# Kernel optimization log

Measured on AMD Instinct MI355X. Metric: run time of the kernel, lower is better.

The kernel has to match this reference:

```python
import jax, jax.numpy as jnp
import numpy as np

B, N, E, D_IN, D_OUT = 8, 8192, 131072, 128, 128
LN_EPS = 1e-5

def setup_inputs() -> dict:
    key = jax.random.key(0)
    k1, k2, k3, k4 = jax.random.split(key, 4)
    node_features = jax.random.normal(k1, (B, N, D_IN), dtype=jnp.float32)
    edge_index = jax.random.randint(k2, (B, 2, E), 0, N, dtype=jnp.int64)
    node_mask = jnp.ones((B, N), dtype=jnp.float32)
    # Linear params (torch Linear: y = x @ W.T + b)
    W = jax.random.normal(k3, (D_OUT, D_IN), dtype=jnp.float32) / np.sqrt(D_IN)
    b = jax.random.normal(k4, (D_OUT,), dtype=jnp.float32) * 0.01
    # LayerNorm params
    gamma = jnp.ones((D_OUT,), dtype=jnp.float32)
    beta = jnp.zeros((D_OUT,), dtype=jnp.float32)
    return {"node_features": node_features, "edge_index": edge_index,
            "node_mask": node_mask, "W": W, "b": b, "gamma": gamma, "beta": beta}

def reference(node_features, edge_index, node_mask, W, b, gamma, beta):
    max_nodes = node_features.shape[1]
    h = jnp.einsum('bni,oi->bno', node_features, W) + b  # [B,N,D_OUT]
    def agg_one(hb, eb):
        # gather source features then scatter-add into targets
        return jax.ops.segment_sum(hb[eb[0]], eb[1], num_segments=max_nodes)
    aggregated = jax.vmap(agg_one)(h, edge_index)  # [B,N,D_OUT]
    h = h + aggregated / jnp.sqrt(jnp.float32(max_nodes))
    # dropout is identity in eval mode
    mu = jnp.mean(h, axis=-1, keepdims=True)
    var = jnp.mean((h - mu) ** 2, axis=-1, keepdims=True)
    h = (h - mu) * jax.lax.rsqrt(var + LN_EPS) * gamma + beta
    h = jax.nn.relu(h)
    return h * node_mask[..., None]
```

## Files before the change

kernel.cpp:

```cpp
#include <hip/hip_runtime.h>

#define B_ 8
#define N_ 8192
#define E_ 131072
#define D_ 128
#define M_ (B_ * N_)
#define SLOTS 64
#define NCH 32
#define CHE (E_ / NCH)
constexpr float INV_SQRT_N = 0.011048543456039806f;
constexpr float LN_EPS_C = 1e-5f;

typedef __attribute__((ext_vector_type(8))) short bf16x8;
typedef __attribute__((ext_vector_type(4))) float f32x4;
typedef __attribute__((ext_vector_type(4))) float f32x4v;
typedef __attribute__((ext_vector_type(4))) unsigned u32x4;

static __device__ __forceinline__ unsigned short f2bf(float f) {
  unsigned u = __float_as_uint(f);
  u += 0x7fffu + ((u >> 16) & 1u);
  return (unsigned short)(u >> 16);
}
static __device__ __forceinline__ float bflo(unsigned u) {
  return __uint_as_float(u << 16);
}
static __device__ __forceinline__ float bfhi(unsigned u) {
  return __uint_as_float(u & 0xffff0000u);
}
static __device__ __forceinline__ bf16x8 cvt8v(const f32x4v a, const f32x4v b) {
  bf16x8 r;
  r[0] = (short)f2bf(a.x); r[1] = (short)f2bf(a.y);
  r[2] = (short)f2bf(a.z); r[3] = (short)f2bf(a.w);
  r[4] = (short)f2bf(b.x); r[5] = (short)f2bf(b.y);
  r[6] = (short)f2bf(b.z); r[7] = (short)f2bf(b.w);
  return r;
}

__global__ __launch_bounds__(256, 2) void gemm_count_kernel(
    const float* __restrict__ X, const float* __restrict__ W,
    const float* __restrict__ bias, const int* __restrict__ eidx,
    unsigned short* __restrict__ histc, unsigned short* __restrict__ rankb,
    unsigned short* __restrict__ hb) {
  __shared__ unsigned hist[N_];
  if (blockIdx.x < 256) {
    const int wave = threadIdx.x >> 6;
    const int lane = threadIdx.x & 63;
    const int m16 = lane & 15;
    const int q = lane >> 4;
    const int hf = wave & 1;
    const int ng = wave >> 1;

    bf16x8 wf[4][4];
#pragma unroll
    for (int kt4 = 0; kt4 < 4; ++kt4) {
#pragma unroll
      for (int tt = 0; tt < 4; ++tt) {
        const float* wr = W + (size_t)(hf * 64 + tt * 16 + m16) * D_ +
                          kt4 * 32 + q * 8;
        wf[kt4][tt] = cvt8v(*(const f32x4v*)wr, *(const f32x4v*)(wr + 4));
      }
    }

    const int bi = blockIdx.x;
    const int nbase0 = (bi & 7) * N_ + (bi >> 3) * 256 + ng * 128;
#pragma unroll 2
    for (int s = 0; s < 8; ++s) {
      const int nbase = nbase0 + s * 16;
      const float* xrow = X + (size_t)(nbase + m16) * D_;

      f32x4 acc[4];
#pragma unroll
      for (int tt = 0; tt < 4; ++tt) acc[tt] = (f32x4){0.f, 0.f, 0.f, 0.f};

#pragma unroll
      for (int kt4 = 0; kt4 < 4; ++kt4) {
        const f32x4v xa = __builtin_nontemporal_load(
            (const f32x4v*)(xrow + kt4 * 32 + q * 8));
        const f32x4v xb = __builtin_nontemporal_load(
            (const f32x4v*)(xrow + kt4 * 32 + q * 8 + 4));
        const bf16x8 xf = cvt8v(xa, xb);
#pragma unroll
        for (int tt = 0; tt < 4; ++tt) {
          acc[tt] = __builtin_amdgcn_mfma_f32_16x16x32_bf16(wf[kt4][tt], xf,
                                                            acc[tt], 0, 0, 0);
        }
      }

      const size_t orow = (size_t)(nbase + m16) * D_;
#pragma unroll
      for (int tt = 0; tt < 4; ++tt) {
        const int f0 = hf * 64 + tt * 16 + q * 4;
        const float4 b4 = *(const float4*)&bias[f0];
        uint2 uu;
        uu.x = (unsigned)f2bf(acc[tt][0] + b4.x) |
               ((unsigned)f2bf(acc[tt][1] + b4.y) << 16);
        uu.y = (unsigned)f2bf(acc[tt][2] + b4.z) |
               ((unsigned)f2bf(acc[tt][3] + b4.w) << 16);
        *(uint2*)(hb + orow + f0) = uu;
      }
    }
  } else {
    const int f = blockIdx.x - 256;
    const int b = f & 7;
    const int c = f >> 3;
    const int t = threadIdx.x;

#pragma unroll
    for (int i = 0; i < N_ / 256; ++i) hist[t + i * 256] = 0u;
    __syncthreads();

    const int* __restrict__ tgtp = eidx + b * 2 * E_ + E_ + c * CHE;
    unsigned short* __restrict__ rnk = rankb + (size_t)b * E_ + c * CHE;
#pragma unroll
    for (int k = 0; k < 4; ++k) {
      const int4 tv = *(const int4*)(tgtp + t * 16 + k * 4);
      const unsigned r0 = atomicAdd(&hist[tv.x], 1u);
      const unsigned r1 = atomicAdd(&hist[tv.y], 1u);
      const unsigned r2 = atomicAdd(&hist[tv.z], 1u);
      const unsigned r3 = atomicAdd(&hist[tv.w], 1u);
      uint2 rr;
      rr.x = (r0 & 0xffffu) | (r1 << 16);
      rr.y = (r2 & 0xffffu) | (r3 << 16);
      *(uint2*)(rnk + t * 16 + k * 4) = rr;
    }
    __syncthreads();

    unsigned* dst = (unsigned*)(histc + ((size_t)b * NCH + c) * N_);
#pragma unroll
    for (int i = 0; i < N_ / 512; ++i) {
      const int j = t + i * 256;
      const unsigned lo = hist[2 * j];
      const unsigned hi = hist[2 * j + 1];
      dst[j] = (lo & 0xffffu) | (hi << 16);
    }
  }
}

__global__ __launch_bounds__(256, 8) void prefix_kernel(
    unsigned short* __restrict__ histc, int* __restrict__ cnt) {
  const int b = blockIdx.x & 7;
  const int nb = blockIdx.x >> 3;
  const int n = nb * 256 + threadIdx.x;
  unsigned short* base = histc + (size_t)b * NCH * N_ + n;
  unsigned short v[NCH];
#pragma unroll
  for (int c = 0; c < NCH; ++c) v[c] = base[(size_t)c * N_];
  unsigned run = 0;
#pragma unroll
  for (int c = 0; c < NCH; ++c) {
    const unsigned x = v[c];
    base[(size_t)c * N_] = (unsigned short)run;
    run += x;
  }
  cnt[b * N_ + n] = (int)run;
}

__global__ __launch_bounds__(256, 8) void place_kernel(
    const int* __restrict__ eidx, const unsigned short* __restrict__ histc,
    const unsigned short* __restrict__ rankb,
    unsigned short* __restrict__ bucket) {
  const int b = blockIdx.x & 7;
  const int pos = blockIdx.x >> 3;
  const int c = pos >> 2;
  const int t = threadIdx.x;
  const int e0 = pos * 1024 + t * 4;

  const int* __restrict__ srcp = eidx + b * 2 * E_;
  const int4 tv = *(const int4*)(srcp + E_ + e0);
  const int4 sv = *(const int4*)(srcp + e0);
  const uint2 rr = *(const uint2*)(rankb + (size_t)b * E_ + e0);
  const unsigned short* __restrict__ basep = histc + ((size_t)b * NCH + c) * N_;
  unsigned short* __restrict__ bkt = bucket + (size_t)b * N_ * SLOTS;

  const unsigned p0 = (unsigned)basep[tv.x] + (rr.x & 0xffffu);
  const unsigned p1 = (unsigned)basep[tv.y] + (rr.x >> 16);
  const unsigned p2 = (unsigned)basep[tv.z] + (rr.y & 0xffffu);
  const unsigned p3 = (unsigned)basep[tv.w] + (rr.y >> 16);
  if (p0 < SLOTS) bkt[(size_t)tv.x * SLOTS + p0] = (unsigned short)sv.x;
  if (p1 < SLOTS) bkt[(size_t)tv.y * SLOTS + p1] = (unsigned short)sv.y;
  if (p2 < SLOTS) bkt[(size_t)tv.z * SLOTS + p2] = (unsigned short)sv.z;
  if (p3 < SLOTS) bkt[(size_t)tv.w * SLOTS + p3] = (unsigned short)sv.w;
}

__global__ __launch_bounds__(256, 8) void gather_finalize_kernel(
    const unsigned short* __restrict__ hb, const unsigned short* __restrict__ bucket,
    const int* __restrict__ cnt, const float* __restrict__ mask,
    const float* __restrict__ gamma, const float* __restrict__ beta,
    float* __restrict__ out) {
  const int bid = blockIdx.x;
  const int batch = bid & 7;
  const int wave = threadIdx.x >> 6;
  const int lane = threadIdx.x & 63;
  const int g = lane >> 4;
  const int c = lane & 15;
  const int r = (bid >> 3) * 16 + wave * 4 + g;
  const int row = batch * N_ + r;

  const u32x4* hub4 = (const u32x4*)hb + (size_t)batch * N_ * 16;

  const int deg = min(cnt[row], SLOTS);
  const uint2 su = *(const uint2*)&bucket[(size_t)row * SLOTS + c * 4];
  const u32x4 ur = hub4[r * 16 + c];
  const float m = mask[row];

  float a[8];
#pragma unroll
  for (int k = 0; k < 8; ++k) a[k] = 0.f;

  for (int jb = 0; jb < deg; jb += 8) {
    const int L = jb >> 2;
    const unsigned w0 = (unsigned)__shfl((int)su.x, L, 16);
    const unsigned w1 = (unsigned)__shfl((int)su.y, L, 16);
    const unsigned w2 = (unsigned)__shfl((int)su.x, L + 1, 16);
    const unsigned w3 = (unsigned)__shfl((int)su.y, L + 1, 16);
    const int idx[8] = {(int)(w0 & 0xffff), (int)(w0 >> 16),
                        (int)(w1 & 0xffff), (int)(w1 >> 16),
                        (int)(w2 & 0xffff), (int)(w2 >> 16),
                        (int)(w3 & 0xffff), (int)(w3 >> 16)};
    u32x4 v[8];
#pragma unroll
    for (int i = 0; i < 8; ++i) {
      const bool val = (jb + i) < deg;
      const int id = val ? idx[i] : 0;
      u32x4 tv = hub4[id * 16 + c];
      if (!val) tv = (u32x4){0u, 0u, 0u, 0u};
      v[i] = tv;
    }
#pragma unroll
    for (int i = 0; i < 8; ++i) {
      a[0] += bflo(v[i].x); a[1] += bfhi(v[i].x);
      a[2] += bflo(v[i].y); a[3] += bfhi(v[i].y);
      a[4] += bflo(v[i].z); a[5] += bfhi(v[i].z);
      a[6] += bflo(v[i].w); a[7] += bfhi(v[i].w);
    }
  }

  float x[8];
  x[0] = bflo(ur.x) + a[0] * INV_SQRT_N;
  x[1] = bfhi(ur.x) + a[1] * INV_SQRT_N;
  x[2] = bflo(ur.y) + a[2] * INV_SQRT_N;
  x[3] = bfhi(ur.y) + a[3] * INV_SQRT_N;
  x[4] = bflo(ur.z) + a[4] * INV_SQRT_N;
  x[5] = bfhi(ur.z) + a[5] * INV_SQRT_N;
  x[6] = bflo(ur.w) + a[6] * INV_SQRT_N;
  x[7] = bfhi(ur.w) + a[7] * INV_SQRT_N;

  float s0 = 0.f, ss = 0.f;
#pragma unroll
  for (int k = 0; k < 8; ++k) {
    s0 += x[k];
    ss += x[k] * x[k];
  }
#pragma unroll
  for (int o = 8; o >= 1; o >>= 1) {
    s0 += __shfl_xor(s0, o, 16);
    ss += __shfl_xor(ss, o, 16);
  }
  const float mu = s0 * (1.f / 128.f);
  float var = ss * (1.f / 128.f) - mu * mu;
  var = var < 0.f ? 0.f : var;
  const float rstd = rsqrtf(var + LN_EPS_C);

  const f32x4v g0 = *((const f32x4v*)gamma + c * 2);
  const f32x4v g1 = *((const f32x4v*)gamma + c * 2 + 1);
  const f32x4v b0 = *((const f32x4v*)beta + c * 2);
  const f32x4v b1 = *((const f32x4v*)beta + c * 2 + 1);

  f32x4v o0, o1;
  o0.x = (x[0] - mu) * rstd * g0.x + b0.x;
  o0.y = (x[1] - mu) * rstd * g0.y + b0.y;
  o0.z = (x[2] - mu) * rstd * g0.z + b0.z;
  o0.w = (x[3] - mu) * rstd * g0.w + b0.w;
  o1.x = (x[4] - mu) * rstd * g1.x + b1.x;
  o1.y = (x[5] - mu) * rstd * g1.y + b1.y;
  o1.z = (x[6] - mu) * rstd * g1.z + b1.z;
  o1.w = (x[7] - mu) * rstd * g1.w + b1.w;
  o0.x = (o0.x > 0.f ? o0.x : 0.f) * m;
  o0.y = (o0.y > 0.f ? o0.y : 0.f) * m;
  o0.z = (o0.z > 0.f ? o0.z : 0.f) * m;
  o0.w = (o0.w > 0.f ? o0.w : 0.f) * m;
  o1.x = (o1.x > 0.f ? o1.x : 0.f) * m;
  o1.y = (o1.y > 0.f ? o1.y : 0.f) * m;
  o1.z = (o1.z > 0.f ? o1.z : 0.f) * m;
  o1.w = (o1.w > 0.f ? o1.w : 0.f) * m;

  f32x4v* op = (f32x4v*)out + (size_t)row * 32 + c * 2;
  __builtin_nontemporal_store(o0, op);
  __builtin_nontemporal_store(o1, op + 1);
}

extern "C" void kernel_launch(void* const* d_in, const int* in_sizes, int n_in,
                              void* d_out, int out_size, void* d_ws,
                              size_t ws_size, hipStream_t stream) {
  const float* X = (const float*)d_in[0];
  const int* eidx = (const int*)d_in[1];
  const float* mask = (const float*)d_in[2];
  const float* W = (const float*)d_in[3];
  const float* bias = (const float*)d_in[4];
  const float* gamma = (const float*)d_in[5];
  const float* beta = (const float*)d_in[6];
  float* out = (float*)d_out;

  unsigned short* hb = (unsigned short*)d_ws;
  unsigned short* bucket = hb + (size_t)M_ * D_;
  int* cnt = (int*)(bucket + (size_t)M_ * SLOTS);
  unsigned short* rankb = (unsigned short*)(cnt + M_);
  unsigned short* histc = (unsigned short*)out;

  gemm_count_kernel<<<512, 256, 0, stream>>>(X, W, bias, eidx, histc, rankb,
                                             hb);
  prefix_kernel<<<256, 256, 0, stream>>>(histc, cnt);
  place_kernel<<<1024, 256, 0, stream>>>(eidx, histc, rankb, bucket);
  gather_finalize_kernel<<<M_ / 16, 256, 0, stream>>>(hb, bucket, cnt, mask,
                                                      gamma, beta, out);
}
```

Measured before the change: 153.6 us.

## Split feature table into column halves and gather each half in separate passes

The GEMM now writes the bf16 hidden features as two column-half planes of 64 features each, and the gather/finalize step becomes two kernels, one per half. The first pass writes partial pre-norm values and LayerNorm sums to workspace, and the second combines them and applies the normalization. The goal is a per-batch gather working set small enough to stay in cache, cutting random-gather traffic to HBM. The cost is an extra launch, reading the bucket indices twice, and a round trip of fp32 intermediates and stats through memory.

```diff
diff --git a/kernel.cpp b/kernel.cpp
--- a/kernel.cpp
+++ b/kernel.cpp
@@ -14,7 +14,6 @@
 typedef __attribute__((ext_vector_type(8))) short bf16x8;
 typedef __attribute__((ext_vector_type(4))) float f32x4;
 typedef __attribute__((ext_vector_type(4))) float f32x4v;
-typedef __attribute__((ext_vector_type(4))) unsigned u32x4;
 
 static __device__ __forceinline__ unsigned short f2bf(float f) {
   unsigned u = __float_as_uint(f);
@@ -63,6 +62,7 @@
 
     const int bi = blockIdx.x;
     const int nbase0 = (bi & 7) * N_ + (bi >> 3) * 256 + ng * 128;
+    unsigned short* __restrict__ hp = hb + (size_t)hf * M_ * 64;
 #pragma unroll 2
     for (int s = 0; s < 8; ++s) {
       const int nbase = nbase0 + s * 16;
@@ -86,7 +86,7 @@
         }
       }
 
-      const size_t orow = (size_t)(nbase + m16) * D_;
+      const size_t prow = (size_t)(nbase + m16) * 64;
 #pragma unroll
       for (int tt = 0; tt < 4; ++tt) {
         const int f0 = hf * 64 + tt * 16 + q * 4;
@@ -96,7 +96,7 @@
                ((unsigned)f2bf(acc[tt][1] + b4.y) << 16);
         uu.y = (unsigned)f2bf(acc[tt][2] + b4.z) |
                ((unsigned)f2bf(acc[tt][3] + b4.w) << 16);
-        *(uint2*)(hb + orow + f0) = uu;
+        *(uint2*)(hp + prow + tt * 16 + q * 4) = uu;
       }
     }
   } else {
@@ -182,11 +182,10 @@
   if (p3 < SLOTS) bkt[(size_t)tv.w * SLOTS + p3] = (unsigned short)sv.w;
 }
 
-__global__ __launch_bounds__(256, 8) void gather_finalize_kernel(
-    const unsigned short* __restrict__ hb, const unsigned short* __restrict__ bucket,
-    const int* __restrict__ cnt, const float* __restrict__ mask,
-    const float* __restrict__ gamma, const float* __restrict__ beta,
-    float* __restrict__ out) {
+__global__ __launch_bounds__(256, 8) void gather_half0_kernel(
+    const unsigned short* __restrict__ hb0,
+    const unsigned short* __restrict__ bucket, const int* __restrict__ cnt,
+    float* __restrict__ xh, float2* __restrict__ stats) {
   const int bid = blockIdx.x;
   const int batch = bid & 7;
   const int wave = threadIdx.x >> 6;
@@ -196,17 +195,13 @@
   const int r = (bid >> 3) * 16 + wave * 4 + g;
   const int row = batch * N_ + r;
 
-  const u32x4* hub4 = (const u32x4*)hb + (size_t)batch * N_ * 16;
+  const uint2* hub2 = (const uint2*)hb0 + (size_t)batch * N_ * 16;
 
   const int deg = min(cnt[row], SLOTS);
   const uint2 su = *(const uint2*)&bucket[(size_t)row * SLOTS + c * 4];
-  const u32x4 ur = hub4[r * 16 + c];
-  const float m = mask[row];
-
-  float a[8];
-#pragma unroll
-  for (int k = 0; k < 8; ++k) a[k] = 0.f;
-
+  const uint2 ur = hub2[r * 16 + c];
+
+  float a[4] = {0.f, 0.f, 0.f, 0.f};
   for (int jb = 0; jb < deg; jb += 8) {
     const int L = jb >> 2;
     const unsigned w0 = (unsigned)__shfl((int)su.x, L, 16);
@@ -217,64 +212,124 @@
                         (int)(w1 & 0xffff), (int)(w1 >> 16),
                         (int)(w2 & 0xffff), (int)(w2 >> 16),
                         (int)(w3 & 0xffff), (int)(w3 >> 16)};
-    u32x4 v[8];
+    uint2 v[8];
 #pragma unroll
     for (int i = 0; i < 8; ++i) {
       const bool val = (jb + i) < deg;
-      const int id = val ? idx[i] : 0;
-      u32x4 tv = hub4[id * 16 + c];
-      if (!val) tv = (u32x4){0u, 0u, 0u, 0u};
+      uint2 tv = hub2[(val ? idx[i] : 0) * 16 + c];
+      if (!val) tv = (uint2){0u, 0u};
       v[i] = tv;
     }
 #pragma unroll
     for (int i = 0; i < 8; ++i) {
       a[0] += bflo(v[i].x); a[1] += bfhi(v[i].x);
       a[2] += bflo(v[i].y); a[3] += bfhi(v[i].y);
-      a[4] += bflo(v[i].z); a[5] += bfhi(v[i].z);
-      a[6] += bflo(v[i].w); a[7] += bfhi(v[i].w);
-    }
-  }
-
-  float x[8];
-  x[0] = bflo(ur.x) + a[0] * INV_SQRT_N;
-  x[1] = bfhi(ur.x) + a[1] * INV_SQRT_N;
-  x[2] = bflo(ur.y) + a[2] * INV_SQRT_N;
-  x[3] = bfhi(ur.y) + a[3] * INV_SQRT_N;
-  x[4] = bflo(ur.z) + a[4] * INV_SQRT_N;
-  x[5] = bfhi(ur.z) + a[5] * INV_SQRT_N;
-  x[6] = bflo(ur.w) + a[6] * INV_SQRT_N;
-  x[7] = bfhi(ur.w) + a[7] * INV_SQRT_N;
-
-  float s0 = 0.f, ss = 0.f;
-#pragma unroll
-  for (int k = 0; k < 8; ++k) {
-    s0 += x[k];
-    ss += x[k] * x[k];
-  }
+    }
+  }
+
+  float4 x;
+  x.x = bflo(ur.x) + a[0] * INV_SQRT_N;
+  x.y = bfhi(ur.x) + a[1] * INV_SQRT_N;
+  x.z = bflo(ur.y) + a[2] * INV_SQRT_N;
+  x.w = bfhi(ur.y) + a[3] * INV_SQRT_N;
+
+  float s0 = x.x + x.y + x.z + x.w;
+  float ss = x.x * x.x + x.y * x.y + x.z * x.z + x.w * x.w;
 #pragma unroll
   for (int o = 8; o >= 1; o >>= 1) {
     s0 += __shfl_xor(s0, o, 16);
     ss += __shfl_xor(ss, o, 16);
   }
+
+  *(float4*)(xh + (size_t)row * 64 + c * 4) = x;
+  if (c == 0) stats[row] = make_float2(s0, ss);
+}
+
+__global__ __launch_bounds__(256, 8) void gather_half1_kernel(
+    const unsigned short* __restrict__ hb1,
+    const unsigned short* __restrict__ bucket, const int* __restrict__ cnt,
+    const float* __restrict__ mask, const float* __restrict__ gamma,
+    const float* __restrict__ beta, const float* __restrict__ xh,
+    const float2* __restrict__ stats, float* __restrict__ out) {
+  const int bid = blockIdx.x;
+  const int batch = bid & 7;
+  const int wave = threadIdx.x >> 6;
+  const int lane = threadIdx.x & 63;
+  const int g = lane >> 4;
+  const int c = lane & 15;
+  const int r = (bid >> 3) * 16 + wave * 4 + g;
+  const int row = batch * N_ + r;
+
+  const uint2* hub2 = (const uint2*)hb1 + (size_t)batch * N_ * 16;
+
+  const int deg = min(cnt[row], SLOTS);
+  const uint2 su = *(const uint2*)&bucket[(size_t)row * SLOTS + c * 4];
+  const uint2 ur = hub2[r * 16 + c];
+  const float m = mask[row];
+
+  float a[4] = {0.f, 0.f, 0.f, 0.f};
+  for (int jb = 0; jb < deg; jb += 8) {
+    const int L = jb >> 2;
+    const unsigned w0 = (unsigned)__shfl((int)su.x, L, 16);
+    const unsigned w1 = (unsigned)__shfl((int)su.y, L, 16);
+    const unsigned w2 = (unsigned)__shfl((int)su.x, L + 1, 16);
+    const unsigned w3 = (unsigned)__shfl((int)su.y, L + 1, 16);
+    const int idx[8] = {(int)(w0 & 0xffff), (int)(w0 >> 16),
+                        (int)(w1 & 0xffff), (int)(w1 >> 16),
+                        (int)(w2 & 0xffff), (int)(w2 >> 16),
+                        (int)(w3 & 0xffff), (int)(w3 >> 16)};
+    uint2 v[8];
+#pragma unroll
+    for (int i = 0; i < 8; ++i) {
+      const bool val = (jb + i) < deg;
+      uint2 tv = hub2[(val ? idx[i] : 0) * 16 + c];
+      if (!val) tv = (uint2){0u, 0u};
+      v[i] = tv;
+    }
+#pragma unroll
+    for (int i = 0; i < 8; ++i) {
+      a[0] += bflo(v[i].x); a[1] += bfhi(v[i].x);
+      a[2] += bflo(v[i].y); a[3] += bfhi(v[i].y);
+    }
+  }
+
+  float4 x1;
+  x1.x = bflo(ur.x) + a[0] * INV_SQRT_N;
+  x1.y = bfhi(ur.x) + a[1] * INV_SQRT_N;
+  x1.z = bflo(ur.y) + a[2] * INV_SQRT_N;
+  x1.w = bfhi(ur.y) + a[3] * INV_SQRT_N;
+
+  float s0 = x1.x + x1.y + x1.z + x1.w;
+  float ss = x1.x * x1.x + x1.y * x1.y + x1.z * x1.z + x1.w * x1.w;
+#pragma unroll
+  for (int o = 8; o >= 1; o >>= 1) {
+    s0 += __shfl_xor(s0, o, 16);
+    ss += __shfl_xor(ss, o, 16);
+  }
+  const float2 st = stats[row];
+  s0 += st.x;
+  ss += st.y;
+
   const float mu = s0 * (1.f / 128.f);
   float var = ss * (1.f / 128.f) - mu * mu;
   var = var < 0.f ? 0.f : var;
   const float rstd = rsqrtf(var + LN_EPS_C);
 
-  const f32x4v g0 = *((const f32x4v*)gamma + c * 2);
-  const f32x4v g1 = *((const f32x4v*)gamma + c * 2 + 1);
-  const f32x4v b0 = *((const f32x4v*)beta + c * 2);
-  const f32x4v b1 = *((const f32x4v*)beta + c * 2 + 1);
+  const float4 x0 = *(const float4*)(xh + (size_t)row * 64 + c * 4);
+  const float4 g0 = ((const float4*)gamma)[c];
+  const float4 g1 = ((const float4*)gamma)[16 + c];
+  const float4 b0 = ((const float4*)beta)[c];
+  const float4 b1 = ((const float4*)beta)[16 + c];
 
   f32x4v o0, o1;
-  o0.x = (x[0] - mu) * rstd * g0.x + b0.x;
-  o0.y = (x[1] - mu) * rstd * g0.y + b0.y;
-  o0.z = (x[2] - mu) * rstd * g0.z + b0.z;
-  o0.w = (x[3] - mu) * rstd * g0.w + b0.w;
-  o1.x = (x[4] - mu) * rstd * g1.x + b1.x;
-  o1.y = (x[5] - mu) * rstd * g1.y + b1.y;
-  o1.z = (x[6] - mu) * rstd * g1.z + b1.z;
-  o1.w = (x[7] - mu) * rstd * g1.w + b1.w;
+  o0.x = (x0.x - mu) * rstd * g0.x + b0.x;
+  o0.y = (x0.y - mu) * rstd * g0.y + b0.y;
+  o0.z = (x0.z - mu) * rstd * g0.z + b0.z;
+  o0.w = (x0.w - mu) * rstd * g0.w + b0.w;
+  o1.x = (x1.x - mu) * rstd * g1.x + b1.x;
+  o1.y = (x1.y - mu) * rstd * g1.y + b1.y;
+  o1.z = (x1.z - mu) * rstd * g1.z + b1.z;
+  o1.w = (x1.w - mu) * rstd * g1.w + b1.w;
   o0.x = (o0.x > 0.f ? o0.x : 0.f) * m;
   o0.y = (o0.y > 0.f ? o0.y : 0.f) * m;
   o0.z = (o0.z > 0.f ? o0.z : 0.f) * m;
@@ -284,9 +339,9 @@
   o1.z = (o1.z > 0.f ? o1.z : 0.f) * m;
   o1.w = (o1.w > 0.f ? o1.w : 0.f) * m;
 
-  f32x4v* op = (f32x4v*)out + (size_t)row * 32 + c * 2;
-  __builtin_nontemporal_store(o0, op);
-  __builtin_nontemporal_store(o1, op + 1);
+  f32x4v* op = (f32x4v*)out + (size_t)row * 32;
+  __builtin_nontemporal_store(o0, op + c);
+  __builtin_nontemporal_store(o1, op + 16 + c);
 }
 
 extern "C" void kernel_launch(void* const* d_in, const int* in_sizes, int n_in,
@@ -302,15 +357,19 @@
   float* out = (float*)d_out;
 
   unsigned short* hb = (unsigned short*)d_ws;
-  unsigned short* bucket = hb + (size_t)M_ * D_;
+  unsigned short* bucket = hb + (size_t)2 * M_ * 64;
   int* cnt = (int*)(bucket + (size_t)M_ * SLOTS);
   unsigned short* rankb = (unsigned short*)(cnt + M_);
+  float* xh = (float*)(rankb + (size_t)B_ * E_);
+  float2* stats = (float2*)(xh + (size_t)M_ * 64);
   unsigned short* histc = (unsigned short*)out;
 
   gemm_count_kernel<<<512, 256, 0, stream>>>(X, W, bias, eidx, histc, rankb,
                                              hb);
   prefix_kernel<<<256, 256, 0, stream>>>(histc, cnt);
   place_kernel<<<1024, 256, 0, stream>>>(eidx, histc, rankb, bucket);
-  gather_finalize_kernel<<<M_ / 16, 256, 0, stream>>>(hb, bucket, cnt, mask,
-                                                      gamma, beta, out);
-}
+  gather_half0_kernel<<<M_ / 16, 256, 0, stream>>>(hb, bucket, cnt, xh, stats);
+  gather_half1_kernel<<<M_ / 16, 256, 0, stream>>>(hb + (size_t)M_ * 64,
+                                                   bucket, cnt, mask, gamma,
+                                                   beta, xh, stats, out);
+}
```

New measurement: 161.9 us. +5.4%, slower.

## Fuse count, prefix and place kernels with grid-wide software barriers

Applied to the files above, without the earlier changes.

Merges the histogram/count, prefix-scan and placement kernels into one launch that also holds the GEMM blocks. The 256 counting blocks synchronise among themselves with atomic-counter spin barriers before the scan and placement phases, and a memset resets the counters beforehand. This removes two kernel launches and the gaps between them. It depends on all 256 counting blocks being co-resident: 512 blocks at 2 per CU with 32KB LDS each could deadlock if residency is insufficient, and the memset adds its own small launch.

```diff
diff --git a/kernel.cpp b/kernel.cpp
--- a/kernel.cpp
+++ b/kernel.cpp
@@ -36,15 +36,34 @@
   return r;
 }
 
-__global__ __launch_bounds__(256, 2) void gemm_count_kernel(
+static __device__ __forceinline__ void sub_barrier(unsigned* bar,
+                                                   unsigned nblk) {
+  __syncthreads();
+  if (threadIdx.x == 0) {
+    __threadfence();
+    atomicAdd(bar, 1u);
+    while (__hip_atomic_load(bar, __ATOMIC_RELAXED,
+                             __HIP_MEMORY_SCOPE_AGENT) < nblk) {
+      __builtin_amdgcn_s_sleep(1);
+    }
+  }
+  __syncthreads();
+  __threadfence();
+}
+
+__global__ __launch_bounds__(256, 2) void fused_front_kernel(
     const float* __restrict__ X, const float* __restrict__ W,
     const float* __restrict__ bias, const int* __restrict__ eidx,
     unsigned short* __restrict__ histc, unsigned short* __restrict__ rankb,
-    unsigned short* __restrict__ hb) {
+    unsigned short* __restrict__ hb, int* __restrict__ cnt,
+    unsigned short* __restrict__ bucket, unsigned* __restrict__ bar) {
   __shared__ unsigned hist[N_];
-  if (blockIdx.x < 256) {
-    const int wave = threadIdx.x >> 6;
-    const int lane = threadIdx.x & 63;
+  const int bid = blockIdx.x;
+  const int t = threadIdx.x;
+
+  if (bid < 256) {
+    const int wave = t >> 6;
+    const int lane = t & 63;
     const int m16 = lane & 15;
     const int q = lane >> 4;
     const int hf = wave & 1;
@@ -61,8 +80,7 @@
       }
     }
 
-    const int bi = blockIdx.x;
-    const int nbase0 = (bi & 7) * N_ + (bi >> 3) * 256 + ng * 128;
+    const int nbase0 = (bid & 7) * N_ + (bid >> 3) * 256 + ng * 128;
 #pragma unroll 2
     for (int s = 0; s < 8; ++s) {
       const int nbase = nbase0 + s * 16;
@@ -99,12 +117,14 @@
         *(uint2*)(hb + orow + f0) = uu;
       }
     }
-  } else {
-    const int f = blockIdx.x - 256;
-    const int b = f & 7;
-    const int c = f >> 3;
-    const int t = threadIdx.x;
-
+    return;
+  }
+
+  const int f = bid - 256;
+  const int b = f & 7;
+  const int c = f >> 3;
+
+  {
 #pragma unroll
     for (int i = 0; i < N_ / 256; ++i) hist[t + i * 256] = 0u;
     __syncthreads();
@@ -134,52 +154,51 @@
       dst[j] = (lo & 0xffffu) | (hi << 16);
     }
   }
-}
-
-__global__ __launch_bounds__(256, 8) void prefix_kernel(
-    unsigned short* __restrict__ histc, int* __restrict__ cnt) {
-  const int b = blockIdx.x & 7;
-  const int nb = blockIdx.x >> 3;
-  const int n = nb * 256 + threadIdx.x;
-  unsigned short* base = histc + (size_t)b * NCH * N_ + n;
-  unsigned short v[NCH];
-#pragma unroll
-  for (int c = 0; c < NCH; ++c) v[c] = base[(size_t)c * N_];
-  unsigned run = 0;
-#pragma unroll
-  for (int c = 0; c < NCH; ++c) {
-    const unsigned x = v[c];
-    base[(size_t)c * N_] = (unsigned short)run;
-    run += x;
-  }
-  cnt[b * N_ + n] = (int)run;
-}
-
-__global__ __launch_bounds__(256, 8) void place_kernel(
-    const int* __restrict__ eidx, const unsigned short* __restrict__ histc,
-    const unsigned short* __restrict__ rankb,
-    unsigned short* __restrict__ bucket) {
-  const int b = blockIdx.x & 7;
-  const int pos = blockIdx.x >> 3;
-  const int c = pos >> 2;
-  const int t = threadIdx.x;
-  const int e0 = pos * 1024 + t * 4;
-
-  const int* __restrict__ srcp = eidx + b * 2 * E_;
-  const int4 tv = *(const int4*)(srcp + E_ + e0);
-  const int4 sv = *(const int4*)(srcp + e0);
-  const uint2 rr = *(const uint2*)(rankb + (size_t)b * E_ + e0);
-  const unsigned short* __restrict__ basep = histc + ((size_t)b * NCH + c) * N_;
-  unsigned short* __restrict__ bkt = bucket + (size_t)b * N_ * SLOTS;
-
-  const unsigned p0 = (unsigned)basep[tv.x] + (rr.x & 0xffffu);
-  const unsigned p1 = (unsigned)basep[tv.y] + (rr.x >> 16);
-  const unsigned p2 = (unsigned)basep[tv.z] + (rr.y & 0xffffu);
-  const unsigned p3 = (unsigned)basep[tv.w] + (rr.y >> 16);
-  if (p0 < SLOTS) bkt[(size_t)tv.x * SLOTS + p0] = (unsigned short)sv.x;
-  if (p1 < SLOTS) bkt[(size_t)tv.y * SLOTS + p1] = (unsigned short)sv.y;
-  if (p2 < SLOTS) bkt[(size_t)tv.z * SLOTS + p2] = (unsigned short)sv.z;
-  if (p3 < SLOTS) bkt[(size_t)tv.w * SLOTS + p3] = (unsigned short)sv.w;
+
+  sub_barrier(&bar[0], 256u);
+
+  {
+    const int n = (f >> 3) * 256 + t;
+    unsigned short* base = histc + (size_t)b * NCH * N_ + n;
+    unsigned short v[NCH];
+#pragma unroll
+    for (int cc = 0; cc < NCH; ++cc) v[cc] = base[(size_t)cc * N_];
+    unsigned run = 0;
+#pragma unroll
+    for (int cc = 0; cc < NCH; ++cc) {
+      const unsigned x = v[cc];
+      base[(size_t)cc * N_] = (unsigned short)run;
+      run += x;
+    }
+    cnt[b * N_ + n] = (int)run;
+  }
+
+  sub_barrier(&bar[1], 256u);
+
+  {
+    const int* __restrict__ srcp = eidx + b * 2 * E_;
+    const int* __restrict__ tgtp = srcp + E_;
+    const unsigned short* __restrict__ basep =
+        histc + ((size_t)b * NCH + c) * N_;
+    const unsigned short* __restrict__ rnk = rankb + (size_t)b * E_ + c * CHE;
+    unsigned short* __restrict__ bkt = bucket + (size_t)b * N_ * SLOTS;
+    const int e0 = c * CHE + t * 16;
+
+#pragma unroll
+    for (int k = 0; k < 4; ++k) {
+      const int4 tv = *(const int4*)(tgtp + e0 + k * 4);
+      const int4 sv = *(const int4*)(srcp + e0 + k * 4);
+      const uint2 rr = *(const uint2*)(rnk + t * 16 + k * 4);
+      const unsigned p0 = (unsigned)basep[tv.x] + (rr.x & 0xffffu);
+      const unsigned p1 = (unsigned)basep[tv.y] + (rr.x >> 16);
+      const unsigned p2 = (unsigned)basep[tv.z] + (rr.y & 0xffffu);
+      const unsigned p3 = (unsigned)basep[tv.w] + (rr.y >> 16);
+      if (p0 < SLOTS) bkt[(size_t)tv.x * SLOTS + p0] = (unsigned short)sv.x;
+      if (p1 < SLOTS) bkt[(size_t)tv.y * SLOTS + p1] = (unsigned short)sv.y;
+      if (p2 < SLOTS) bkt[(size_t)tv.z * SLOTS + p2] = (unsigned short)sv.z;
+      if (p3 < SLOTS) bkt[(size_t)tv.w * SLOTS + p3] = (unsigned short)sv.w;
+    }
+  }
 }
 
 __global__ __launch_bounds__(256, 8) void gather_finalize_kernel(
@@ -305,12 +324,12 @@
   unsigned short* bucket = hb + (size_t)M_ * D_;
   int* cnt = (int*)(bucket + (size_t)M_ * SLOTS);
   unsigned short* rankb = (unsigned short*)(cnt + M_);
+  unsigned* bar = (unsigned*)(rankb + (size_t)B_ * E_);
   unsigned short* histc = (unsigned short*)out;
 
-  gemm_count_kernel<<<512, 256, 0, stream>>>(X, W, bias, eidx, histc, rankb,
-                                             hb);
-  prefix_kernel<<<256, 256, 0, stream>>>(histc, cnt);
-  place_kernel<<<1024, 256, 0, stream>>>(eidx, histc, rankb, bucket);
+  (void)hipMemsetAsync(bar, 0, 2 * sizeof(unsigned), stream);
+  fused_front_kernel<<<512, 256, 0, stream>>>(X, W, bias, eidx, histc, rankb,
+                                              hb, cnt, bucket, bar);
   gather_finalize_kernel<<<M_ / 16, 256, 0, stream>>>(hb, bucket, cnt, mask,
                                                       gamma, beta, out);
 }
```

After: 244.3 us. 1.59x slower.
